# Optimization experiments

Hardware: AMD Instinct MI355X
Metric: run time of the kernel (lower is better)

The kernel has to match this reference:

```python
import jax, jax.numpy as jnp
import numpy as np

N_QUBITS = 8
IN_DIM = 256
HID = 8  # must equal N_QUBITS (broadcasting in the original cell requires it)
B = 512
T = 512


def _zmat(n):
    # [2^n, n] matrix of Pauli-Z eigenvalues per basis state / wire (wire 0 = MSB,
    # matching torchquantum's state ordering).
    idx = np.arange(2 ** n)
    bits = (idx[:, None] >> (n - 1 - np.arange(n))) & 1
    return jnp.asarray(1.0 - 2.0 * bits, dtype=jnp.float32)


def _apply_rx(state, theta, w):
    # state: [M, 2, ..., 2] complex64, theta: [M] real. RX(theta) on wire w.
    st = jnp.moveaxis(state, w + 1, 1)
    a0, a1 = st[:, 0], st[:, 1]
    shp = (-1,) + (1,) * (a0.ndim - 1)
    c = jnp.cos(theta * 0.5).reshape(shp).astype(state.dtype)
    s = (-1j * jnp.sin(theta * 0.5)).reshape(shp).astype(state.dtype)
    new = jnp.stack([c * a0 + s * a1, s * a0 + c * a1], axis=1)
    return jnp.moveaxis(new, 1, w + 1)


def _cnot(state, c, t):
    # CNOT control c, target t on state [M, 2, ..., 2].
    s0 = jax.lax.index_in_dim(state, 0, axis=c + 1, keepdims=False)
    s1 = jax.lax.index_in_dim(state, 1, axis=c + 1, keepdims=False)
    t_ax = t + 1 if t < c else t  # target axis index after control axis removed
    s1 = jnp.flip(s1, axis=t_ax)
    return jnp.stack([s0, s1], axis=c + 1)


def _circuit(angles, zmat):
    # angles: [M, n] combined RX angles (encoder x + trainable theta, RX angles add).
    # Returns PauliZ expectation per wire: [M, n].
    M, n = angles.shape
    state = jnp.zeros((M,) + (2,) * n, dtype=jnp.complex64)
    state = state.at[(slice(None),) + (0,) * n].set(1.0 + 0j)
    for w in range(n):
        state = _apply_rx(state, angles[:, w], w)
    for w in range(n - 1):
        state = _cnot(state, w, w + 1)
    state = _cnot(state, n - 1, 0)
    sr = state.reshape(M, -1)
    probs = sr.real ** 2 + sr.imag ** 2  # smooth |amp|^2
    return probs @ zmat


def setup_inputs():
    key = jax.random.key(0)
    ks = jax.random.split(key, 10)
    d = IN_DIM + HID
    sc = 1.0 / np.sqrt(d)
    inp = {"inputs": jax.random.normal(ks[0], (B, T, IN_DIM), dtype=jnp.float32)}
    for i, name in enumerate(["f", "i", "g", "o"]):
        inp["W" + name] = jax.random.uniform(ks[1 + 2 * i], (N_QUBITS, d), minval=-sc, maxval=sc, dtype=jnp.float32)
        inp["b" + name] = jax.random.uniform(ks[2 + 2 * i], (N_QUBITS,), minval=-sc, maxval=sc, dtype=jnp.float32)
    inp["thetas"] = jax.random.normal(ks[9], (4, N_QUBITS), dtype=jnp.float32) * 0.1
    return inp


def reference(inputs, Wf, bf, Wi, bi, Wg, bg, Wo, bo, thetas):
    zmat = _zmat(N_QUBITS)
    bsz = inputs.shape[0]
    hx0 = jnp.zeros((bsz, HID), inputs.dtype)
    cx0 = jnp.zeros((bsz, HID), inputs.dtype)
    W = jnp.stack([Wf, Wi, Wg, Wo])       # [4, n, d]
    bias = jnp.stack([bf, bi, bg, bo])    # [4, n]

    def step(carry, x_t):
        hx, cx = carry
        comb = jnp.concatenate([x_t, hx], axis=1)  # [B, D+H]
        # fc angles + trainable RX angle (RX rotations on same wire compose additively)
        ang = jnp.einsum('gnd,bd->gbn', W, comb) + bias[:, None, :] + thetas[:, None, :]
        m = _circuit(ang.reshape(4 * bsz, N_QUBITS), zmat).reshape(4, bsz, N_QUBITS)
        f = jax.nn.sigmoid(m[0])
        i = jax.nn.sigmoid(m[1])
        g = jnp.tanh(m[2])
        o = jax.nn.sigmoid(m[3])
        cx2 = f * cx + i * g
        hx2 = o * jnp.tanh(cx2)
        return (hx2, cx2), hx2

    (hx, cx), outs = jax.lax.scan(step, (hx0, cx0), jnp.swapaxes(inputs, 0, 1))
    return jnp.swapaxes(outs, 0, 1), hx, cx
```

## Files before the change

kernel.cpp:

```cpp
#include <hip/hip_runtime.h>


#define BQ   512
#define TT   512
#define IND  256
#define PRE_OFF 8704


__global__ void prep_kernel(const float* __restrict__ Wf, const float* __restrict__ bf,
                            const float* __restrict__ Wi, const float* __restrict__ bi,
                            const float* __restrict__ Wg, const float* __restrict__ bg,
                            const float* __restrict__ Wo, const float* __restrict__ bo,
                            const float* __restrict__ th, float* __restrict__ wsf) {
    const float* W[4]    = {Wf, Wi, Wg, Wo};
    const float* bias[4] = {bf, bi, bg, bo};
    int d = threadIdx.x;
    for (int g = 0; g < 4; g++)
        for (int n = 0; n < 8; n++)
            wsf[d * 32 + g * 8 + n] = W[g][n * 264 + d];
    if (d < 32) {
        int g = d >> 3, n = d & 7;
        for (int j = 0; j < 8; j++)
            wsf[8192 + d * 8 + j] = W[g][n * 264 + 256 + j];
        wsf[8448 + d] = bias[g][n] + th[d];
    }
}

__global__ __launch_bounds__(256) void pre_gemm(const float* __restrict__ x,
                                                const float* __restrict__ wsf,
                                                float* __restrict__ pre) {
    const int bt = blockIdx.x * 256 + threadIdx.x;
    const float4* xr = (const float4*)(x + (size_t)bt * IND);
    const float* cvec = wsf + 8448;
    float acc[32];
#pragma unroll
    for (int k = 0; k < 32; k++) acc[k] = cvec[k];
    for (int dq = 0; dq < 64; dq++) {
        float4 xv = xr[dq];
        const float* wr = wsf + dq * 128;
#pragma unroll
        for (int k = 0; k < 32; k++) acc[k] = fmaf(xv.x, wr[k], acc[k]);
#pragma unroll
        for (int k = 0; k < 32; k++) acc[k] = fmaf(xv.y, wr[32 + k], acc[k]);
#pragma unroll
        for (int k = 0; k < 32; k++) acc[k] = fmaf(xv.z, wr[64 + k], acc[k]);
#pragma unroll
        for (int k = 0; k < 32; k++) acc[k] = fmaf(xv.w, wr[96 + k], acc[k]);
    }
    const int b = bt >> 9, t = bt & 511, t4 = t >> 2, tm = t & 3;
    float* dst = pre + ((size_t)(b * 128 + t4)) * 128 + tm;
#pragma unroll
    for (int k = 0; k < 32; k++) dst[k * 4] = acc[k];
}

#define SWZ(x, imm) __int_as_float(__builtin_amdgcn_ds_swizzle(__float_as_int(x), (imm)))

template <int CTRL>
__device__ __forceinline__ float dpp_shr(float x) {
    return __int_as_float(__builtin_amdgcn_update_dpp(
        0, __float_as_int(x), CTRL, 0xF, 0xF, true));
}

__global__ __launch_bounds__(64) void recur(const float* __restrict__ wsf,
                                            float* __restrict__ out) {
    const int lane = threadIdx.x;
    const int l32  = lane & 31;
    const int half = lane >> 5;
    const int b    = blockIdx.x * 2 + half;
    const int g    = l32 >> 3;
    const int n    = l32 & 7;

    float whr[8];
#pragma unroll
    for (int j = 0; j < 8; j++) whr[j] = wsf[8192 + l32 * 8 + j];

    const float4* pp = (const float4*)(wsf + PRE_OFF) + (size_t)b * 128 * 32 + l32;

    float hx[8];
#pragma unroll
    for (int j = 0; j < 8; j++) hx[j] = 0.0f;
    float cx = 0.0f;

    float4 bufA = pp[0];
    float4 bufB = pp[32];

    float* outp = out + (size_t)b * TT * 8 + n;
    const float L2E = 1.4426950408889634f;

    for (int t4 = 0; t4 < 128; t4++) {
        float4 cur = (t4 & 1) ? bufB : bufA;
        int nx = (t4 + 2 < 128) ? (t4 + 2) : 127;
        if (t4 & 1) bufB = pp[(size_t)nx * 32];
        else        bufA = pp[(size_t)nx * 32];
        float pv4[4] = {cur.x, cur.y, cur.z, cur.w};
#pragma unroll
        for (int tm = 0; tm < 4; tm++) {
            float ang = pv4[tm];
#pragma unroll
            for (int j = 0; j < 8; j++) ang = fmaf(whr[j], hx[j], ang);
            float c = __cosf(ang);
            float s = (n == 0) ? 1.0f : c;
            { float v = dpp_shr<0x111>(s); s = (n >= 1) ? s * v : s; }
            { float v = dpp_shr<0x112>(s); s = (n >= 2) ? s * v : s; }
            { float v = dpp_shr<0x114>(s); s = (n >= 4) ? s * v : s; }
            float c0 = SWZ(c, 0x018);
            float s7 = SWZ(s, 0x0F8);
            float m  = (n == 0) ? s7 : c0 * s;
            float kk  = (g == 2) ? (-2.0f * L2E) : (-L2E);
            float u   = __builtin_amdgcn_rcpf(1.0f + __builtin_amdgcn_exp2f(m * kk));
            float val = (g == 2) ? fmaf(2.0f, u, -1.0f) : u;
            float fv = SWZ(val, 0x007);
            float iv = SWZ(val, 0x107);
            float gv = SWZ(val, 0x207);
            float ov = SWZ(val, 0x307);
            cx = fmaf(fv, cx, iv * gv);
            float t2 = __builtin_amdgcn_exp2f(cx * (-2.0f * L2E));
            float th = fmaf(2.0f, __builtin_amdgcn_rcpf(1.0f + t2), -1.0f);
            float hxn = ov * th;
            if (l32 < 8) outp[(t4 * 4 + tm) * 8] = hxn;
            hx[0] = SWZ(hxn, 0x018);
            hx[1] = SWZ(hxn, 0x038);
            hx[2] = SWZ(hxn, 0x058);
            hx[3] = SWZ(hxn, 0x078);
            hx[4] = SWZ(hxn, 0x098);
            hx[5] = SWZ(hxn, 0x0B8);
            hx[6] = SWZ(hxn, 0x0D8);
            hx[7] = SWZ(hxn, 0x0F8);
        }
    }
    if (l32 < 8) {
        out[(size_t)BQ * TT * 8 + b * 8 + n]            = hx[n];
        out[(size_t)BQ * TT * 8 + BQ * 8 + b * 8 + n]   = cx;
    }
}

extern "C" void kernel_launch(void* const* d_in, const int* in_sizes, int n_in,
                              void* d_out, int out_size, void* d_ws, size_t ws_size,
                              hipStream_t stream) {
    const float* x  = (const float*)d_in[0];
    const float* Wf = (const float*)d_in[1];
    const float* bf = (const float*)d_in[2];
    const float* Wi = (const float*)d_in[3];
    const float* bi = (const float*)d_in[4];
    const float* Wg = (const float*)d_in[5];
    const float* bg = (const float*)d_in[6];
    const float* Wo = (const float*)d_in[7];
    const float* bo = (const float*)d_in[8];
    const float* th = (const float*)d_in[9];
    float* wsf = (float*)d_ws;
    float* out = (float*)d_out;

    prep_kernel<<<1, 256, 0, stream>>>(Wf, bf, Wi, bi, Wg, bg, Wo, bo, th, wsf);
    pre_gemm<<<(BQ * TT) / 256, 256, 0, stream>>>(x, wsf, wsf + PRE_OFF);
    recur<<<BQ / 2, 64, 0, stream>>>(wsf, out);
}
```

Baseline: 552.8 us.

## Stage x tiles through LDS with coalesced loads and register prefetch in pre_gemm

In pre_gemm, each thread used to read its own 1 KB row of x, so lanes in a wavefront touched addresses 1 KB apart. Now the block loads 32-column chunks of 256 rows with coalesced float4 reads into a padded shared-memory tile, and each thread then reads its own row from LDS. The next chunk is prefetched into registers while the current one is computed. This adds two barriers per chunk, about 36 KB of LDS per block, and extra staging registers, which may lower occupancy.

```diff
diff --git a/kernel.cpp b/kernel.cpp
--- a/kernel.cpp
+++ b/kernel.cpp
@@ -26,27 +26,63 @@
     }
 }
 
+#define CHUNK 32
+#define NCH   8
+#define PITCH 36
+
 __global__ __launch_bounds__(256) void pre_gemm(const float* __restrict__ x,
                                                 const float* __restrict__ wsf,
                                                 float* __restrict__ pre) {
-    const int bt = blockIdx.x * 256 + threadIdx.x;
-    const float4* xr = (const float4*)(x + (size_t)bt * IND);
+    __shared__ float tile[256 * PITCH];
+    const int tid  = threadIdx.x;
+    const int row0 = blockIdx.x * 256;
+    const int lrow = tid >> 3;
+    const int lc4  = tid & 7;
+
     const float* cvec = wsf + 8448;
     float acc[32];
 #pragma unroll
     for (int k = 0; k < 32; k++) acc[k] = cvec[k];
-    for (int dq = 0; dq < 64; dq++) {
-        float4 xv = xr[dq];
-        const float* wr = wsf + dq * 128;
+
+    float4 stg[8];
 #pragma unroll
-        for (int k = 0; k < 32; k++) acc[k] = fmaf(xv.x, wr[k], acc[k]);
+    for (int i = 0; i < 8; i++) {
+        int r = i * 32 + lrow;
+        stg[i] = *(const float4*)(x + (size_t)(row0 + r) * IND + lc4 * 4);
+    }
+
+    for (int c = 0; c < NCH; c++) {
+        __syncthreads();
 #pragma unroll
-        for (int k = 0; k < 32; k++) acc[k] = fmaf(xv.y, wr[32 + k], acc[k]);
+        for (int i = 0; i < 8; i++) {
+            int r = i * 32 + lrow;
+            *(float4*)&tile[r * PITCH + lc4 * 4] = stg[i];
+        }
+        __syncthreads();
+        if (c + 1 < NCH) {
 #pragma unroll
-        for (int k = 0; k < 32; k++) acc[k] = fmaf(xv.z, wr[64 + k], acc[k]);
+            for (int i = 0; i < 8; i++) {
+                int r = i * 32 + lrow;
+                stg[i] = *(const float4*)(x + (size_t)(row0 + r) * IND + (c + 1) * CHUNK + lc4 * 4);
+            }
+        }
+        const float* wbase = wsf + c * CHUNK * 32;
 #pragma unroll
-        for (int k = 0; k < 32; k++) acc[k] = fmaf(xv.w, wr[96 + k], acc[k]);
+        for (int q = 0; q < 8; q++) {
+            float4 xv = *(const float4*)&tile[tid * PITCH + q * 4];
+            const float* wr = wbase + q * 128;
+#pragma unroll
+            for (int k = 0; k < 32; k++) acc[k] = fmaf(xv.x, wr[k], acc[k]);
+#pragma unroll
+            for (int k = 0; k < 32; k++) acc[k] = fmaf(xv.y, wr[32 + k], acc[k]);
+#pragma unroll
+            for (int k = 0; k < 32; k++) acc[k] = fmaf(xv.z, wr[64 + k], acc[k]);
+#pragma unroll
+            for (int k = 0; k < 32; k++) acc[k] = fmaf(xv.w, wr[96 + k], acc[k]);
+        }
     }
+
+    const int bt = row0 + tid;
     const int b = bt >> 9, t = bt & 511, t4 = t >> 2, tm = t & 3;
     float* dst = pre + ((size_t)(b * 128 + t4)) * 128 + tm;
 #pragma unroll
```

Result: no change. 556.9 us (+0.7%).

## Repack recurrence to eight batches per wave with gates held per lane

Applied to the files above, without the earlier changes.

The recurrent kernel now maps one lane to one (batch, wire) pair and computes all four gates in that lane, so each wave handles eight batch rows instead of two. Hidden-state exchange uses DPP quad permutes and a half-mirror in place of ds_swizzle, with the weight columns reordered to match the permuted order. The pre-GEMM output layout is changed to interleave gates per wire so each lane loads one float4 per step, and the prefetch depth goes from two to four. This cuts the number of waves and the cross-lane LDS-swizzle latency on the serial critical path. In exchange each lane does four times the transcendental and FMA work per step, and launch_bounds is removed from pre_gemm.

```diff
diff --git a/kernel.cpp b/kernel.cpp
--- a/kernel.cpp
+++ b/kernel.cpp
@@ -26,9 +26,9 @@
     }
 }
 
-__global__ __launch_bounds__(256) void pre_gemm(const float* __restrict__ x,
-                                                const float* __restrict__ wsf,
-                                                float* __restrict__ pre) {
+__global__ void pre_gemm(const float* __restrict__ x,
+                         const float* __restrict__ wsf,
+                         float* __restrict__ pre) {
     const int bt = blockIdx.x * 256 + threadIdx.x;
     const float4* xr = (const float4*)(x + (size_t)bt * IND);
     const float* cvec = wsf + 8448;
@@ -47,91 +47,100 @@
 #pragma unroll
         for (int k = 0; k < 32; k++) acc[k] = fmaf(xv.w, wr[96 + k], acc[k]);
     }
-    const int b = bt >> 9, t = bt & 511, t4 = t >> 2, tm = t & 3;
-    float* dst = pre + ((size_t)(b * 128 + t4)) * 128 + tm;
+    const int b = bt >> 9, t = bt & 511;
+    float* dst = pre + ((size_t)((b >> 3) * TT + t)) * 256 + (b & 7) * 32;
 #pragma unroll
-    for (int k = 0; k < 32; k++) dst[k * 4] = acc[k];
+    for (int n = 0; n < 8; n++) {
+        float4 v = make_float4(acc[n], acc[8 + n], acc[16 + n], acc[24 + n]);
+        *(float4*)(dst + n * 4) = v;
+    }
 }
 
-#define SWZ(x, imm) __int_as_float(__builtin_amdgcn_ds_swizzle(__float_as_int(x), (imm)))
-
 template <int CTRL>
-__device__ __forceinline__ float dpp_shr(float x) {
+__device__ __forceinline__ float dpp0(float x) {
     return __int_as_float(__builtin_amdgcn_update_dpp(
         0, __float_as_int(x), CTRL, 0xF, 0xF, true));
 }
+#define QP_X1 0xB1
+#define QP_X2 0x4E
+#define QP_X3 0x1B
+#define HMIR  0x141
+#define SHR1  0x111
+#define SHR2  0x112
+#define SHR4  0x114
+#define SHL7  0x107
 
-__global__ __launch_bounds__(64) void recur(const float* __restrict__ wsf,
-                                            float* __restrict__ out) {
-    const int lane = threadIdx.x;
-    const int l32  = lane & 31;
-    const int half = lane >> 5;
-    const int b    = blockIdx.x * 2 + half;
-    const int g    = l32 >> 3;
-    const int n    = l32 & 7;
+__global__ __launch_bounds__(64, 1) void recur(const float* __restrict__ wsf,
+                                               float* __restrict__ out) {
+    const int lane  = threadIdx.x;
+    const int n     = lane & 7;
+    const int b     = blockIdx.x * 8 + (lane >> 3);
+    const float L2E = 1.4426950408889634f;
 
-    float whr[8];
+    const int msk[8] = {0, 1, 2, 3, 7, 6, 5, 4};
+    float w[4][8];
 #pragma unroll
-    for (int j = 0; j < 8; j++) whr[j] = wsf[8192 + l32 * 8 + j];
+    for (int g = 0; g < 4; g++)
+#pragma unroll
+        for (int k = 0; k < 8; k++)
+            w[g][k] = wsf[8192 + (g * 8 + n) * 8 + (n ^ msk[k])];
 
-    const float4* pp = (const float4*)(wsf + PRE_OFF) + (size_t)b * 128 * 32 + l32;
+    const float4* pp = (const float4*)(wsf + PRE_OFF)
+                     + (size_t)blockIdx.x * TT * 64 + lane;
 
-    float hx[8];
+    float hx = 0.0f, cx = 0.0f;
+    float4 buf[4];
 #pragma unroll
-    for (int j = 0; j < 8; j++) hx[j] = 0.0f;
-    float cx = 0.0f;
-
-    float4 bufA = pp[0];
-    float4 bufB = pp[32];
+    for (int i = 0; i < 4; i++) buf[i] = pp[(size_t)i * 64];
 
     float* outp = out + (size_t)b * TT * 8 + n;
-    const float L2E = 1.4426950408889634f;
 
-    for (int t4 = 0; t4 < 128; t4++) {
-        float4 cur = (t4 & 1) ? bufB : bufA;
-        int nx = (t4 + 2 < 128) ? (t4 + 2) : 127;
-        if (t4 & 1) bufB = pp[(size_t)nx * 32];
-        else        bufA = pp[(size_t)nx * 32];
-        float pv4[4] = {cur.x, cur.y, cur.z, cur.w};
+    for (int t = 0; t < TT; t++) {
+        float4 pv = buf[t & 3];
+        if (t + 4 < TT) buf[t & 3] = pp[(size_t)(t + 4) * 64];
+
+        float hm = dpp0<HMIR>(hx);
+        float H[8];
+        H[0] = hx;             H[1] = dpp0<QP_X1>(hx);
+        H[2] = dpp0<QP_X2>(hx); H[3] = dpp0<QP_X3>(hx);
+        H[4] = hm;             H[5] = dpp0<QP_X1>(hm);
+        H[6] = dpp0<QP_X2>(hm); H[7] = dpp0<QP_X3>(hm);
+
+        float ang[4] = {pv.x, pv.y, pv.z, pv.w};
 #pragma unroll
-        for (int tm = 0; tm < 4; tm++) {
-            float ang = pv4[tm];
+        for (int g = 0; g < 4; g++)
 #pragma unroll
-            for (int j = 0; j < 8; j++) ang = fmaf(whr[j], hx[j], ang);
-            float c = __cosf(ang);
-            float s = (n == 0) ? 1.0f : c;
-            { float v = dpp_shr<0x111>(s); s = (n >= 1) ? s * v : s; }
-            { float v = dpp_shr<0x112>(s); s = (n >= 2) ? s * v : s; }
-            { float v = dpp_shr<0x114>(s); s = (n >= 4) ? s * v : s; }
-            float c0 = SWZ(c, 0x018);
-            float s7 = SWZ(s, 0x0F8);
-            float m  = (n == 0) ? s7 : c0 * s;
-            float kk  = (g == 2) ? (-2.0f * L2E) : (-L2E);
-            float u   = __builtin_amdgcn_rcpf(1.0f + __builtin_amdgcn_exp2f(m * kk));
-            float val = (g == 2) ? fmaf(2.0f, u, -1.0f) : u;
-            float fv = SWZ(val, 0x007);
-            float iv = SWZ(val, 0x107);
-            float gv = SWZ(val, 0x207);
-            float ov = SWZ(val, 0x307);
-            cx = fmaf(fv, cx, iv * gv);
-            float t2 = __builtin_amdgcn_exp2f(cx * (-2.0f * L2E));
-            float th = fmaf(2.0f, __builtin_amdgcn_rcpf(1.0f + t2), -1.0f);
-            float hxn = ov * th;
-            if (l32 < 8) outp[(t4 * 4 + tm) * 8] = hxn;
-            hx[0] = SWZ(hxn, 0x018);
-            hx[1] = SWZ(hxn, 0x038);
-            hx[2] = SWZ(hxn, 0x058);
-            hx[3] = SWZ(hxn, 0x078);
-            hx[4] = SWZ(hxn, 0x098);
-            hx[5] = SWZ(hxn, 0x0B8);
-            hx[6] = SWZ(hxn, 0x0D8);
-            hx[7] = SWZ(hxn, 0x0F8);
+            for (int k = 0; k < 8; k++)
+                ang[g] = fmaf(w[g][k], H[k], ang[g]);
+
+        float m[4];
+#pragma unroll
+        for (int g = 0; g < 4; g++) {
+            float c = __cosf(ang[g]);
+            float T = c;
+            { float v = dpp0<SHR1>(T); T = (n >= 1) ? T * v : T; }
+            { float v = dpp0<SHR2>(T); T = (n >= 2) ? T * v : T; }
+            { float v = dpp0<SHR4>(T); T = (n >= 4) ? T * v : T; }
+            float e = (n == 0) ? 1.0f : c;
+            float r = e * dpp0<QP_X1>(e);
+            r = r * dpp0<QP_X2>(r);
+            r = r * dpp0<HMIR>(r);
+            m[g] = (n == 0) ? r : T;
         }
+
+        float f  = __builtin_amdgcn_rcpf(1.0f + __builtin_amdgcn_exp2f(m[0] * (-L2E)));
+        float iv = __builtin_amdgcn_rcpf(1.0f + __builtin_amdgcn_exp2f(m[1] * (-L2E)));
+        float gv = fmaf(2.0f, __builtin_amdgcn_rcpf(1.0f + __builtin_amdgcn_exp2f(m[2] * (-2.0f * L2E))), -1.0f);
+        float ov = __builtin_amdgcn_rcpf(1.0f + __builtin_amdgcn_exp2f(m[3] * (-L2E)));
+
+        cx = fmaf(f, cx, iv * gv);
+        float t2 = __builtin_amdgcn_exp2f(cx * (-2.0f * L2E));
+        hx = ov * fmaf(2.0f, __builtin_amdgcn_rcpf(1.0f + t2), -1.0f);
+
+        outp[(size_t)t * 8] = hx;
     }
-    if (l32 < 8) {
-        out[(size_t)BQ * TT * 8 + b * 8 + n]            = hx[n];
-        out[(size_t)BQ * TT * 8 + BQ * 8 + b * 8 + n]   = cx;
-    }
+    out[(size_t)BQ * TT * 8 + b * 8 + n]          = hx;
+    out[(size_t)BQ * TT * 8 + BQ * 8 + b * 8 + n] = cx;
 }
 
 extern "C" void kernel_launch(void* const* d_in, const int* in_sizes, int n_in,
@@ -152,5 +161,5 @@
 
     prep_kernel<<<1, 256, 0, stream>>>(Wf, bf, Wi, bi, Wg, bg, Wo, bo, th, wsf);
     pre_gemm<<<(BQ * TT) / 256, 256, 0, stream>>>(x, wsf, wsf + PRE_OFF);
-    recur<<<BQ / 2, 64, 0, stream>>>(wsf, out);
+    recur<<<BQ / 8, 64, 0, stream>>>(wsf, out);
 }
```

Measured after the change: 736.9 us. 1.33x slower.
